# Optimization experiments

Measured on AMD Instinct MI355X. Metric: run time of the kernel, lower is better.

Reference implementation:

```python
import jax, jax.numpy as jnp
import numpy as np

B, S, D, OUT = 8, 4096, 2048, 2048
M = 128          # number of saved edit masks
TOP_K = 256
IRR_THRESHOLD = 0.3


def setup_inputs() -> dict:
    key = jax.random.key(0)
    ks = jax.random.split(key, 8)
    x = jax.random.normal(ks[0], (B, S, D), dtype=jnp.float32)
    boundaries = jax.random.randint(ks[1], (B,), 128, S, dtype=jnp.int64)
    weight = jax.random.normal(ks[2], (OUT, D), dtype=jnp.float32) * 0.02
    bias = jax.random.normal(ks[3], (OUT,), dtype=jnp.float32) * 0.02
    new_weight = jax.random.normal(ks[4], (OUT, D), dtype=jnp.float32) * 0.02
    permutation = jax.random.permutation(ks[5], D).astype(jnp.int64)
    # saved masks: exactly TOP_K active dims per stored edit
    scores = jax.random.normal(ks[6], (M, D), dtype=jnp.float32)
    _, idx = jax.lax.top_k(scores, TOP_K)
    saved_masks = jnp.zeros((M, D), dtype=jnp.bool_).at[
        jnp.arange(M)[:, None], idx].set(True)
    bg_mean = jax.random.normal(ks[7], (D,), dtype=jnp.float32) * 0.02
    return {
        "x": x, "boundaries": boundaries, "weight": weight, "bias": bias,
        "new_weight": new_weight, "permutation": permutation,
        "saved_masks": saved_masks, "bg_mean": bg_mean, "top_k": TOP_K,
    }


def reference(x, boundaries, weight, bias, new_weight, permutation,
              saved_masks, bg_mean, top_k):
    bsz, seq_len, dim = x.shape
    # --- aggregate prompt features: masked mean up to boundary, decentered ---
    b = jnp.clip(boundaries, 0, seq_len - 1)
    pos = jnp.arange(seq_len)[None, :]                     # [1, S]
    pmask = (pos <= b[:, None]).astype(x.dtype)            # [B, S]
    denom = jnp.maximum(pmask.sum(axis=1, keepdims=True), 1.0)
    prompt_agg = jnp.einsum('bsd,bs->bd', x, pmask) / denom
    prompt_agg = prompt_agg - bg_mean[None, :]             # mean_decentered
    # --- TopHasher: top-k of |features|, then permute indices ---
    _, top_idx = jax.lax.top_k(jnp.abs(prompt_agg), top_k)  # [B, K]
    active_indices = permutation[top_idx]                   # [B, K]
    active_mask = jnp.zeros((bsz, dim), dtype=jnp.bool_).at[
        jnp.arange(bsz)[:, None], active_indices].set(True)
    # --- retrieve best-overlapping saved mask ---
    overlap = active_mask.astype(jnp.float32) @ saved_masks.T.astype(jnp.float32)
    overlap_ratios = overlap / float(top_k)                 # [B, M]
    best_idx = jnp.argmax(overlap_ratios, axis=1)
    best_overlap = jnp.max(overlap_ratios, axis=1)
    relevant = best_overlap >= IRR_THRESHOLD                # [B]
    best_masks = saved_masks[best_idx]                      # [B, D]
    final_mask = jnp.where(relevant[:, None], best_masks,
                           jnp.zeros_like(best_masks))
    # --- masked new-weight path + original linear ---
    x_hashed = x * final_mask.astype(x.dtype)[:, None, :]
    new_out = jnp.einsum('bsd,od->bso', x_hashed, new_weight)
    orig_out = jnp.einsum('bsd,od->bso', x, weight) + bias
    return orig_out + new_out
```

## Files before the change

### kernel.cpp

```cpp
#include <hip/hip_runtime.h>
#include <stdint.h>

typedef unsigned short u16;
typedef __attribute__((ext_vector_type(4))) float f32x4;
typedef __attribute__((ext_vector_type(4))) u16 u16x4;
typedef __attribute__((ext_vector_type(8))) u16 u16x8;
typedef __attribute__((ext_vector_type(8))) __bf16 bf16x8;

#define B_ 8
#define S_ 4096
#define D_ 2048
#define O_ 2048
#define M_ 128
#define KTOP_ 256

__device__ __forceinline__ u16 f2bf(float f) {
  unsigned int u = __float_as_uint(f);
  u = (u + 0x7FFFu + ((u >> 16) & 1u)) >> 16;
  return (u16)u;
}

__device__ __forceinline__ void g2l16(const void* g, void* l) {
  __builtin_amdgcn_global_load_lds(
      (const __attribute__((address_space(1))) unsigned int*)g,
      (__attribute__((address_space(3))) unsigned int*)l,
      16, 0, 0);
}

__global__ __launch_bounds__(256) void cvt_and_sum(const float* __restrict__ x,
                                                   const int* __restrict__ bnd,
                                                   u16* __restrict__ xb,
                                                   float* __restrict__ sums) {
  const int b = blockIdx.z;
  const int s0 = blockIdx.y * 64;
  const int d = blockIdx.x * 1024 + threadIdx.x * 4;
  const int bclip = min(max(bnd[b], 0), S_ - 1);
  const float* xp = x + (size_t)b * S_ * D_ + (size_t)s0 * D_ + d;
  u16* op = xb + (size_t)b * S_ * D_ + (size_t)s0 * D_ + d;
  const int smax = min(64, bclip + 1 - s0);
  float a0 = 0.f, a1 = 0.f, a2 = 0.f, a3 = 0.f;
  for (int i = 0; i < 64; ++i) {
    f32x4 v = *(const f32x4*)xp;
    u16x4 r;
    r[0] = f2bf(v[0]); r[1] = f2bf(v[1]); r[2] = f2bf(v[2]); r[3] = f2bf(v[3]);
    *(u16x4*)op = r;
    if (i < smax) { a0 += v[0]; a1 += v[1]; a2 += v[2]; a3 += v[3]; }
    xp += D_; op += D_;
  }
  if (smax > 0) {
    atomicAdd(&sums[b * D_ + d + 0], a0);
    atomicAdd(&sums[b * D_ + d + 1], a1);
    atomicAdd(&sums[b * D_ + d + 2], a2);
    atomicAdd(&sums[b * D_ + d + 3], a3);
  }
}

__global__ __launch_bounds__(256) void topk_mask(const float* __restrict__ sums,
                                                 const int* __restrict__ bnd,
                                                 const float* __restrict__ bg_mean,
                                                 const int* __restrict__ perm,
                                                 unsigned char* __restrict__ active) {
  const int b = blockIdx.x;
  __shared__ unsigned int vb[D_];
  __shared__ int hist[256];
  __shared__ int sh_sel, sh_cum;
  const int bclip = min(max(bnd[b], 0), S_ - 1);
  const float denom = (float)(bclip + 1);
  for (int d = threadIdx.x; d < D_; d += 256) {
    float v = fabsf(sums[b * D_ + d] / denom - bg_mean[d]);
    vb[d] = __float_as_uint(v);
  }
  __syncthreads();
  unsigned int prefix = 0;
  int r = KTOP_;
  for (int byte = 3; byte >= 0; --byte) {
    for (int i = threadIdx.x; i < 256; i += 256) hist[i] = 0;
    __syncthreads();
    const unsigned int shift = byte * 8;
    const unsigned int pmask = (byte == 3) ? 0u : (0xFFFFFFFFu << (shift + 8));
    for (int d = threadIdx.x; d < D_; d += 256) {
      unsigned int v = vb[d];
      if ((v & pmask) == prefix) atomicAdd(&hist[(v >> shift) & 0xFF], 1);
    }
    __syncthreads();
    if (threadIdx.x == 0) {
      int cum = 0, sel = 0;
      for (int v = 255; v >= 0; --v) {
        if (cum + hist[v] >= r) { sel = v; break; }
        cum += hist[v];
      }
      sh_sel = sel; sh_cum = cum;
    }
    __syncthreads();
    prefix |= ((unsigned int)sh_sel) << shift;
    r -= sh_cum;
    __syncthreads();
  }
  const unsigned int T = prefix;
  for (int d = threadIdx.x; d < D_; d += 256)
    if (vb[d] > T) active[b * D_ + perm[d]] = 1;
  if (threadIdx.x == 0) {
    int need = r;
    for (int d = 0; d < D_ && need > 0; ++d)
      if (vb[d] == T) { active[b * D_ + perm[d]] = 1; --need; }
  }
}

__global__ __launch_bounds__(128) void select_mask(const unsigned char* __restrict__ active,
                                                   const unsigned char* __restrict__ saved,
                                                   unsigned char* __restrict__ final_mask) {
  const int b = blockIdx.x;
  const int m = threadIdx.x;
  __shared__ __align__(16) unsigned char act[D_];
  __shared__ int cnts[M_];
  __shared__ int sh_best, sh_rel;
  for (int d = m; d < D_; d += 128) act[d] = active[b * D_ + d];
  __syncthreads();
  const unsigned int* sp = (const unsigned int*)(saved + (size_t)m * D_);
  const unsigned int* ap = (const unsigned int*)act;
  int c = 0;
  for (int i = 0; i < D_ / 4; ++i) c += __popc(sp[i] & ap[i]);
  cnts[m] = c;
  __syncthreads();
  if (m == 0) {
    int best = cnts[0], bi = 0;
    for (int i = 1; i < M_; ++i)
      if (cnts[i] > best) { best = cnts[i]; bi = i; }
    sh_best = bi;
    sh_rel = (best >= 77) ? 1 : 0;
  }
  __syncthreads();
  const int bi = sh_best, rel = sh_rel;
  for (int d = m; d < D_; d += 128)
    final_mask[b * D_ + d] = rel ? saved[(size_t)bi * D_ + d] : 0;
}

__global__ __launch_bounds__(256) void build_weff(const float* __restrict__ w,
                                                  const float* __restrict__ nw,
                                                  const unsigned char* __restrict__ fmask,
                                                  u16* __restrict__ weff) {
  int idx = blockIdx.x * 256 + threadIdx.x;
  int bb = idx >> 19;
  int rem = (idx & 524287) << 3;
  int d = rem & (D_ - 1);
  f32x4 w0 = *(const f32x4*)(w + rem);
  f32x4 w1 = *(const f32x4*)(w + rem + 4);
  f32x4 n0 = *(const f32x4*)(nw + rem);
  f32x4 n1 = *(const f32x4*)(nw + rem + 4);
  const unsigned char* mp = fmask + bb * D_ + d;
  u16x8 r;
#pragma unroll
  for (int i = 0; i < 4; ++i) r[i] = f2bf(w0[i] + (mp[i] ? n0[i] : 0.f));
#pragma unroll
  for (int i = 0; i < 4; ++i) r[4 + i] = f2bf(w1[i] + (mp[4 + i] ? n1[i] : 0.f));
  *(u16x8*)(weff + ((size_t)bb << 22) + rem) = r;
}

__global__ __launch_bounds__(256) void gemm_bt(const u16* __restrict__ X,
                                               const u16* __restrict__ W,
                                               const float* __restrict__ bias,
                                               float* __restrict__ out) {
  __shared__ __align__(16) u16 lA[128 * 32];
  __shared__ __align__(16) u16 lB[128 * 32];
  const unsigned int gid = blockIdx.x;
  const int b = gid & 7;
  const int t = gid >> 3;
  const int st = t >> 4, wi = t & 15;
  const int mt = (st & 7) * 4 + (wi & 3);
  const int nt = (st >> 3) * 4 + (wi >> 2);
  const int tid = threadIdx.x;
  const int wave = tid >> 6, lane = tid & 63;
  const int wr = (wave >> 1) * 64, wc = (wave & 1) * 64;
  const int q = lane >> 4, lm = lane & 15;

  const u16* Ab = X + (size_t)b * S_ * D_ + (size_t)(mt * 128) * D_;
  const u16* Bb = W + (size_t)b * O_ * D_ + (size_t)(nt * 128) * D_;

  const int r0 = tid >> 2;
  const int c0 = (tid & 3) * 8;

  f32x4 acc[4][4] = {};

  for (int k0 = 0; k0 < D_; k0 += 32) {
    g2l16(Ab + (size_t)r0 * D_ + k0 + c0, lA + tid * 8);
    g2l16(Ab + (size_t)(r0 + 64) * D_ + k0 + c0, lA + (tid + 256) * 8);
    g2l16(Bb + (size_t)r0 * D_ + k0 + c0, lB + tid * 8);
    g2l16(Bb + (size_t)(r0 + 64) * D_ + k0 + c0, lB + (tid + 256) * 8);
    __syncthreads();

    bf16x8 af[4], bf[4];
#pragma unroll
    for (int i = 0; i < 4; ++i)
      af[i] = *(const bf16x8*)(lA + (wr + i * 16 + lm) * 32 + q * 8);
#pragma unroll
    for (int j = 0; j < 4; ++j)
      bf[j] = *(const bf16x8*)(lB + (wc + j * 16 + lm) * 32 + q * 8);
#pragma unroll
    for (int i = 0; i < 4; ++i)
#pragma unroll
      for (int j = 0; j < 4; ++j)
        acc[i][j] = __builtin_amdgcn_mfma_f32_16x16x32_bf16(af[i], bf[j], acc[i][j], 0, 0, 0);
    __syncthreads();
  }

  const int col0 = nt * 128 + wc + lm;
  const int row0 = mt * 128 + wr + q * 4;
  float bv[4];
#pragma unroll
  for (int j = 0; j < 4; ++j) bv[j] = bias[col0 + j * 16];
#pragma unroll
  for (int i = 0; i < 4; ++i) {
#pragma unroll
    for (int r = 0; r < 4; ++r) {
      const int row = row0 + i * 16 + r;
      float* op = out + (size_t)b * S_ * O_ + (size_t)row * O_;
#pragma unroll
      for (int j = 0; j < 4; ++j) op[col0 + j * 16] = acc[i][j][r] + bv[j];
    }
  }
}

extern "C" void kernel_launch(void* const* d_in, const int* in_sizes, int n_in,
                              void* d_out, int out_size, void* d_ws, size_t ws_size,
                              hipStream_t stream) {
  const float* x          = (const float*)d_in[0];
  const int* boundaries   = (const int*)d_in[1];
  const float* weight     = (const float*)d_in[2];
  const float* bias       = (const float*)d_in[3];
  const float* new_weight = (const float*)d_in[4];
  const int* perm         = (const int*)d_in[5];
  const unsigned char* saved = (const unsigned char*)d_in[6];
  const float* bg_mean    = (const float*)d_in[7];
  float* out = (float*)d_out;

  char* ws = (char*)d_ws;
  const size_t off_xb   = 0;
  const size_t off_weff = off_xb + (size_t)B_ * S_ * D_ * 2;
  const size_t off_sums = off_weff + (size_t)B_ * O_ * D_ * 2;
  const size_t off_act  = off_sums + (size_t)B_ * D_ * 4;
  const size_t off_fin  = off_act + (size_t)B_ * D_;

  u16* xb   = (u16*)(ws + off_xb);
  u16* weff = (u16*)(ws + off_weff);
  float* sums = (float*)(ws + off_sums);
  unsigned char* act = (unsigned char*)(ws + off_act);
  unsigned char* fin = (unsigned char*)(ws + off_fin);

  hipMemsetAsync(ws + off_sums, 0, (size_t)B_ * D_ * 4 + (size_t)B_ * D_, stream);

  cvt_and_sum<<<dim3(D_ / 1024, S_ / 64, B_), 256, 0, stream>>>(x, boundaries, xb, sums);
  topk_mask<<<B_, 256, 0, stream>>>(sums, boundaries, bg_mean, perm, act);
  select_mask<<<B_, 128, 0, stream>>>(act, saved, fin);
  build_weff<<<(B_ * O_ * D_ / 8) / 256, 256, 0, stream>>>(weight, new_weight, fin, weff);
  gemm_bt<<<B_ * 512, 256, 0, stream>>>(xb, weff, bias, out);
}
```

Measured before the change: 1.102 ms.

## Replace GEMM with 256x256 tile, double-buffered swizzled LDS, 8-wave pipelined kernel

The batched GEMM moves from 128x128 tiles with K=32, a single LDS buffer and 4 waves to 256x256 tiles with K=64 and 8 waves. The LDS buffers are double-buffered with an XOR swizzle to avoid bank conflicts. Each K-step is split into four MFMA phases, and global-to-LDS loads for the next stages are issued between them, using explicit vmcnt waits, barriers and setprio to overlap memory with compute. This aims to raise arithmetic intensity and hide load latency, at the cost of 128 KB of LDS, more registers, and fewer blocks (1024).

```diff
diff --git a/kernel.cpp b/kernel.cpp
--- a/kernel.cpp
+++ b/kernel.cpp
@@ -156,66 +156,151 @@
   *(u16x8*)(weff + ((size_t)bb << 22) + rem) = r;
 }
 
-__global__ __launch_bounds__(256) void gemm_bt(const u16* __restrict__ X,
+#define MFMA16(a, b, c) __builtin_amdgcn_mfma_f32_16x16x32_bf16((a), (b), (c), 0, 0, 0)
+
+__global__ __launch_bounds__(512) void gemm256(const u16* __restrict__ X,
                                                const u16* __restrict__ W,
                                                const float* __restrict__ bias,
                                                float* __restrict__ out) {
-  __shared__ __align__(16) u16 lA[128 * 32];
-  __shared__ __align__(16) u16 lB[128 * 32];
+  __shared__ __align__(16) u16 ldsA[2][256][64];
+  __shared__ __align__(16) u16 ldsB[2][256][64];
   const unsigned int gid = blockIdx.x;
   const int b = gid & 7;
   const int t = gid >> 3;
-  const int st = t >> 4, wi = t & 15;
-  const int mt = (st & 7) * 4 + (wi & 3);
-  const int nt = (st >> 3) * 4 + (wi >> 2);
+  const int nt = t & 7;
+  const int mt = t >> 3;
   const int tid = threadIdx.x;
   const int wave = tid >> 6, lane = tid & 63;
-  const int wr = (wave >> 1) * 64, wc = (wave & 1) * 64;
+  const int wm = wave >> 2, wn = wave & 3;
   const int q = lane >> 4, lm = lane & 15;
-
-  const u16* Ab = X + (size_t)b * S_ * D_ + (size_t)(mt * 128) * D_;
-  const u16* Bb = W + (size_t)b * O_ * D_ + (size_t)(nt * 128) * D_;
-
-  const int r0 = tid >> 2;
-  const int c0 = (tid & 3) * 8;
-
-  f32x4 acc[4][4] = {};
-
-  for (int k0 = 0; k0 < D_; k0 += 32) {
-    g2l16(Ab + (size_t)r0 * D_ + k0 + c0, lA + tid * 8);
-    g2l16(Ab + (size_t)(r0 + 64) * D_ + k0 + c0, lA + (tid + 256) * 8);
-    g2l16(Bb + (size_t)r0 * D_ + k0 + c0, lB + tid * 8);
-    g2l16(Bb + (size_t)(r0 + 64) * D_ + k0 + c0, lB + (tid + 256) * 8);
-    __syncthreads();
-
-    bf16x8 af[4], bf[4];
+  const int l7 = lm & 7;
+  const int cA0 = (q ^ l7) << 3;
+  const int tRow = tid >> 3;
+  const int cSw = ((tid & 7) ^ (tRow & 7)) << 3;
+
+  const u16* Ab = X + (size_t)b * S_ * D_ + (size_t)(mt * 256) * D_;
+  const u16* Bb = W + (size_t)b * O_ * D_ + (size_t)(nt * 256) * D_;
+
+#define STAGE_A(p, kt, h) do {                                              \
+    const u16* s_ = Ab + (size_t)((h) * 128 + tRow) * D_ + (kt) * 64 + cSw; \
+    g2l16(s_, &ldsA[p][(h) * 128][0] + tid * 8);                            \
+    g2l16(s_ + (size_t)64 * D_, &ldsA[p][(h) * 128 + 64][0] + tid * 8);     \
+  } while (0)
+#define STAGE_B(p, kt, h) do {                                              \
+    const u16* s_ = Bb + (size_t)((h) * 128 + tRow) * D_ + (kt) * 64 + cSw; \
+    g2l16(s_, &ldsB[p][(h) * 128][0] + tid * 8);                            \
+    g2l16(s_ + (size_t)64 * D_, &ldsB[p][(h) * 128 + 64][0] + tid * 8);     \
+  } while (0)
+
+  f32x4 acc[8][4] = {};
+
+  STAGE_A(0, 0, 0); STAGE_A(0, 0, 1);
+  STAGE_B(0, 0, 0); STAGE_B(0, 0, 1);
+  STAGE_A(1, 1, 0); STAGE_A(1, 1, 1);
+  asm volatile("s_waitcnt vmcnt(4)" ::: "memory");
+  __builtin_amdgcn_s_barrier();
+
+  const int NK = D_ / 64;
+  for (int j = 0; j < NK; ++j) {
+    const int p = j & 1;
+    const u16* la = &ldsA[p][0][0];
+    const u16* lb = &ldsB[p][0][0];
+    bf16x8 af0[4][2], af4[4][2], bf01[2][2], bf23[2][2];
+
+#pragma unroll
+    for (int i = 0; i < 4; ++i) {
+      const u16* rp = la + (wm * 128 + i * 16 + lm) * 64;
+      af0[i][0] = *(const bf16x8*)(rp + cA0);
+      af0[i][1] = *(const bf16x8*)(rp + (cA0 ^ 32));
+    }
+#pragma unroll
+    for (int n = 0; n < 2; ++n) {
+      const u16* rp = lb + (wn * 64 + n * 16 + lm) * 64;
+      bf01[n][0] = *(const bf16x8*)(rp + cA0);
+      bf01[n][1] = *(const bf16x8*)(rp + (cA0 ^ 32));
+    }
+    if (j + 1 < NK) STAGE_B(p ^ 1, j + 1, 0);
+    __builtin_amdgcn_s_barrier();
+    __builtin_amdgcn_s_setprio(1);
 #pragma unroll
     for (int i = 0; i < 4; ++i)
-      af[i] = *(const bf16x8*)(lA + (wr + i * 16 + lm) * 32 + q * 8);
-#pragma unroll
-    for (int j = 0; j < 4; ++j)
-      bf[j] = *(const bf16x8*)(lB + (wc + j * 16 + lm) * 32 + q * 8);
+#pragma unroll
+      for (int n = 0; n < 2; ++n) {
+        acc[i][n] = MFMA16(af0[i][0], bf01[n][0], acc[i][n]);
+        acc[i][n] = MFMA16(af0[i][1], bf01[n][1], acc[i][n]);
+      }
+    __builtin_amdgcn_s_setprio(0);
+    __builtin_amdgcn_s_barrier();
+
+#pragma unroll
+    for (int i = 0; i < 4; ++i) {
+      const u16* rp = la + (wm * 128 + 64 + i * 16 + lm) * 64;
+      af4[i][0] = *(const bf16x8*)(rp + cA0);
+      af4[i][1] = *(const bf16x8*)(rp + (cA0 ^ 32));
+    }
+    if (j + 1 < NK) STAGE_B(p ^ 1, j + 1, 1);
+    __builtin_amdgcn_s_barrier();
+    __builtin_amdgcn_s_setprio(1);
 #pragma unroll
     for (int i = 0; i < 4; ++i)
 #pragma unroll
-      for (int j = 0; j < 4; ++j)
-        acc[i][j] = __builtin_amdgcn_mfma_f32_16x16x32_bf16(af[i], bf[j], acc[i][j], 0, 0, 0);
-    __syncthreads();
-  }
-
-  const int col0 = nt * 128 + wc + lm;
-  const int row0 = mt * 128 + wr + q * 4;
+      for (int n = 0; n < 2; ++n) {
+        acc[4 + i][n] = MFMA16(af4[i][0], bf01[n][0], acc[4 + i][n]);
+        acc[4 + i][n] = MFMA16(af4[i][1], bf01[n][1], acc[4 + i][n]);
+      }
+    __builtin_amdgcn_s_setprio(0);
+    __builtin_amdgcn_s_barrier();
+
+#pragma unroll
+    for (int n = 0; n < 2; ++n) {
+      const u16* rp = lb + (wn * 64 + (2 + n) * 16 + lm) * 64;
+      bf23[n][0] = *(const bf16x8*)(rp + cA0);
+      bf23[n][1] = *(const bf16x8*)(rp + (cA0 ^ 32));
+    }
+    if (j + 2 < NK) STAGE_A(p, j + 2, 0);
+    __builtin_amdgcn_s_barrier();
+    __builtin_amdgcn_s_setprio(1);
+#pragma unroll
+    for (int i = 0; i < 4; ++i)
+#pragma unroll
+      for (int n = 0; n < 2; ++n) {
+        acc[4 + i][2 + n] = MFMA16(af4[i][0], bf23[n][0], acc[4 + i][2 + n]);
+        acc[4 + i][2 + n] = MFMA16(af4[i][1], bf23[n][1], acc[4 + i][2 + n]);
+      }
+    __builtin_amdgcn_s_setprio(0);
+    __builtin_amdgcn_s_barrier();
+
+    if (j + 2 < NK) STAGE_A(p, j + 2, 1);
+    if (j < NK - 2) asm volatile("s_waitcnt vmcnt(4)" ::: "memory");
+    else            asm volatile("s_waitcnt vmcnt(0)" ::: "memory");
+    __builtin_amdgcn_s_barrier();
+    __builtin_amdgcn_s_setprio(1);
+#pragma unroll
+    for (int i = 0; i < 4; ++i)
+#pragma unroll
+      for (int n = 0; n < 2; ++n) {
+        acc[i][2 + n] = MFMA16(af0[i][0], bf23[n][0], acc[i][2 + n]);
+        acc[i][2 + n] = MFMA16(af0[i][1], bf23[n][1], acc[i][2 + n]);
+      }
+    __builtin_amdgcn_s_setprio(0);
+    __builtin_amdgcn_s_barrier();
+  }
+#undef STAGE_A
+#undef STAGE_B
+
+  const int colbase = nt * 256 + wn * 64 + lm;
+  const int rowbase = mt * 256 + wm * 128 + q * 4;
   float bv[4];
 #pragma unroll
-  for (int j = 0; j < 4; ++j) bv[j] = bias[col0 + j * 16];
-#pragma unroll
-  for (int i = 0; i < 4; ++i) {
-#pragma unroll
-    for (int r = 0; r < 4; ++r) {
-      const int row = row0 + i * 16 + r;
-      float* op = out + (size_t)b * S_ * O_ + (size_t)row * O_;
-#pragma unroll
-      for (int j = 0; j < 4; ++j) op[col0 + j * 16] = acc[i][j][r] + bv[j];
+  for (int n = 0; n < 4; ++n) bv[n] = bias[colbase + n * 16];
+  float* outb = out + (size_t)b * S_ * O_;
+#pragma unroll
+  for (int i = 0; i < 8; ++i) {
+#pragma unroll
+    for (int rr = 0; rr < 4; ++rr) {
+      float* op = outb + (size_t)(rowbase + i * 16 + rr) * O_ + colbase;
+#pragma unroll
+      for (int n = 0; n < 4; ++n) op[n * 16] = acc[i][n][rr] + bv[n];
     }
   }
 }
@@ -252,5 +337,5 @@
   topk_mask<<<B_, 256, 0, stream>>>(sums, boundaries, bg_mean, perm, act);
   select_mask<<<B_, 128, 0, stream>>>(act, saved, fin);
   build_weff<<<(B_ * O_ * D_ / 8) / 256, 256, 0, stream>>>(weight, new_weight, fin, weff);
-  gemm_bt<<<B_ * 512, 256, 0, stream>>>(xb, weff, bias, out);
-}
+  gemm256<<<B_ * 128, 512, 0, stream>>>(xb, weff, bias, out);
+}
```

Measured after the change: 1.026 ms. 6.9% less time.
